# Performance work log

Hardware: AMD Instinct MI355X
Metric: run time of the kernel (lower is better)

Reference implementation:

```python
import jax, jax.numpy as jnp
import numpy as np

N = 100000          # num_nodes
E = 1250000         # num_edges
H = 64              # node_hidden_size
T = 2               # num_rounds


def setup_inputs() -> dict:
    key = jax.random.key(0)
    ks = jax.random.split(key, 10)
    s = 0.1  # init scale for weights
    return {
        "x": jax.random.normal(ks[0], (N, H), dtype=jnp.float32),
        "edge_index": jax.random.randint(ks[1], (2, E), 0, N, dtype=jnp.int64),
        "edge_attr": jax.random.normal(ks[2], (E, 1), dtype=jnp.float32),
        # message layers: Linear(2H+1 -> H), one per round
        "msg_W": jax.random.normal(ks[3], (T, H, 2 * H + 1), dtype=jnp.float32) * s,
        "msg_b": jax.random.normal(ks[4], (T, H), dtype=jnp.float32) * s,
        # GRUCell params, gate order (r, z, n) as in torch
        "gru_Wih": jax.random.normal(ks[5], (T, 3 * H, H), dtype=jnp.float32) * s,
        "gru_bih": jax.random.normal(ks[6], (T, 3 * H), dtype=jnp.float32) * s,
        "gru_Whh": jax.random.normal(ks[7], (T, 3 * H, H), dtype=jnp.float32) * s,
        "gru_bhh": jax.random.normal(ks[8], (T, 3 * H), dtype=jnp.float32) * s,
    }


def _gru_cell(inp, h, Wih, bih, Whh, bhh):
    # torch.nn.GRUCell math, gate order r, z, n
    gi = inp @ Wih.T + bih   # [N, 3H]
    gh = h @ Whh.T + bhh     # [N, 3H]
    i_r, i_z, i_n = jnp.split(gi, 3, axis=1)
    h_r, h_z, h_n = jnp.split(gh, 3, axis=1)
    r = jax.nn.sigmoid(i_r + h_r)
    z = jax.nn.sigmoid(i_z + h_z)
    n = jnp.tanh(i_n + r * h_n)
    return (1.0 - z) * n + z * h


def reference(x, edge_index, edge_attr, msg_W, msg_b, gru_Wih, gru_bih, gru_Whh, gru_bhh):
    row, col = edge_index[0], edge_index[1]
    num_rounds = msg_W.shape[0]
    for t in range(num_rounds):
        src = x[row]    # [E, H]
        dest = x[col]   # [E, H]
        m_input = jnp.concatenate([dest, src, edge_attr], axis=1)  # [E, 2H+1]
        messages = m_input @ msg_W[t].T + msg_b[t]                 # [E, H]
        agg = jax.ops.segment_sum(messages, row, num_segments=x.shape[0])  # [N, H]
        x = _gru_cell(agg, x, gru_Wih[t], gru_bih[t], gru_Whh[t], gru_bhh[t])
    return x
```

## Files before the change

### kernel.cpp

```cpp
#include <hip/hip_runtime.h>
#include <hip/hip_bf16.h>
#include <hip/hip_fp16.h>

#define H 64

typedef __attribute__((ext_vector_type(8))) short short8;
typedef __attribute__((ext_vector_type(4))) float float4v;

__device__ __forceinline__ float lane_bcast(float v, int k) {
    return __int_as_float(__builtin_amdgcn_readlane(__float_as_int(v), k));
}
__device__ __forceinline__ short f2bf_bits(float f) {
    union { __hip_bfloat16 b; short s; } u;
    u.b = __float2bfloat16(f);
    return u.s;
}
__device__ __forceinline__ float bf2f(unsigned short s) {
    union { unsigned int u; float f; } v;
    v.u = ((unsigned int)s) << 16;
    return v.f;
}
__device__ __forceinline__ void split8(const float* __restrict__ p,
                                       short8& hi, short8& lo) {
    float4v f0 = *(const float4v*)p;
    float4v f1 = *(const float4v*)(p + 4);
#pragma unroll
    for (int j = 0; j < 8; j++) {
        float f = (j < 4) ? f0[j] : f1[j - 4];
        short h = f2bf_bits(f);
        float fh = bf2f((unsigned short)h);
        hi[j] = h;
        lo[j] = f2bf_bits(f - fh);
    }
}
__device__ __forceinline__ void zero8(short8& hi, short8& lo) {
#pragma unroll
    for (int j = 0; j < 8; j++) { hi[j] = 0; lo[j] = 0; }
}

#define MFMA(a, b, c) __builtin_amdgcn_mfma_f32_16x16x32_bf16(a, b, c, 0, 0, 0)

__global__ __launch_bounds__(64) void prep_msg(
    const float* __restrict__ msg_W, short* __restrict__ frag)
{
    const int slot = blockIdx.x & 15, t = blockIdx.x >> 4, lane = threadIdx.x;
    const int tile = slot >> 1, ks = slot & 1;
    const float* W = msg_W + (size_t)t * H * 129;
    const int wrow = (tile & 3) * 16 + (lane & 15);
    const int coff = (tile < 4) ? 0 : 64;
    const int kq = (lane >> 4) * 8;
    short8 hi, lo;
    split8(W + (size_t)wrow * 129 + coff + ks * 32 + kq, hi, lo);
    short8* out = (short8*)(frag + (size_t)t * 16384);
    out[slot * 64 + lane] = hi;
    out[16 * 64 + slot * 64 + lane] = lo;
}

__global__ __launch_bounds__(64) void prep_gru(
    const float* __restrict__ Wih, const float* __restrict__ Whh,
    short* __restrict__ frag)
{
    const int slot = blockIdx.x % 48, t = blockIdx.x / 48, lane = threadIdx.x;
    const int tile = slot >> 1, ks = slot & 1;
    const int kq = (lane >> 4) * 8;
    const float* Wp = (tile < 12)
        ? (Wih + (size_t)t * 192 * H + ((size_t)(tile * 16 + (lane & 15))) * H)
        : (Whh + (size_t)t * 192 * H + ((size_t)((tile - 12) * 16 + (lane & 15))) * H);
    short8 hi, lo;
    split8(Wp + ks * 32 + kq, hi, lo);
    short8* out = (short8*)(frag + (size_t)t * 49152);
    out[slot * 64 + lane] = hi;
    out[48 * 64 + slot * 64 + lane] = lo;
}

__global__ __launch_bounds__(256) void count_kernel(
    const int* __restrict__ row, int* __restrict__ deg,
    int* __restrict__ lpos, int E)
{
    int e = blockIdx.x * 256 + threadIdx.x;
    if (e < E) lpos[e] = atomicAdd(&deg[row[e]], 1);
}

__global__ __launch_bounds__(256) void scan_block(
    const int* __restrict__ deg, int* __restrict__ offsets,
    int* __restrict__ block_sums, int N)
{
    __shared__ int s[256];
    int tid = threadIdx.x, gid = blockIdx.x * 256 + tid;
    int v = (gid < N) ? deg[gid] : 0;
    s[tid] = v; __syncthreads();
    for (int off = 1; off < 256; off <<= 1) {
        int t = (tid >= off) ? s[tid - off] : 0;
        __syncthreads();
        s[tid] += t;
        __syncthreads();
    }
    if (gid < N) offsets[gid] = s[tid] - v;
    if (tid == 255) block_sums[blockIdx.x] = s[255];
}

__global__ __launch_bounds__(512) void scan_sums(int* __restrict__ block_sums, int nb)
{
    __shared__ int s[512];
    int tid = threadIdx.x;
    int v = (tid < nb) ? block_sums[tid] : 0;
    s[tid] = v; __syncthreads();
    for (int off = 1; off < 512; off <<= 1) {
        int t = (tid >= off) ? s[tid - off] : 0;
        __syncthreads();
        s[tid] += t;
        __syncthreads();
    }
    if (tid < nb) block_sums[tid] = s[tid] - v;
}

__global__ __launch_bounds__(256) void scan_add(
    int* __restrict__ offsets, const int* __restrict__ block_sums, int N, int E)
{
    int gid = blockIdx.x * 256 + threadIdx.x;
    if (gid < N) offsets[gid] += block_sums[blockIdx.x];
    if (gid == 0) offsets[N] = E;
}

__global__ __launch_bounds__(256) void scatter_kernel(
    const int* __restrict__ row, const int* __restrict__ col,
    const float* __restrict__ attr, const int* __restrict__ offsets,
    const int* __restrict__ lpos, int2* __restrict__ edata, int E)
{
    int e = blockIdx.x * 256 + threadIdx.x;
    if (e < E) {
        int p = offsets[row[e]] + lpos[e];
        int2 v;
        v.x = col[e];
        v.y = __float_as_int(attr[e]);
        edata[p] = v;
    }
}

#define NSLOT(mt, ks, hl) ((((mt) * 2 + (ks)) * 2 + (hl)))
__global__ __launch_bounds__(256) void node_transform_mfma(
    const float* __restrict__ x, const short* __restrict__ frag,
    const float* __restrict__ b, const int* __restrict__ deg,
    __half* __restrict__ xd, float* __restrict__ agg, int N)
{
    __shared__ short8 afrag[16 * 64];
    const int tid = threadIdx.x, lane = tid & 63, q = tid >> 6;
    const int base = blockIdx.x * 64;
    const int arow = lane & 15;
    const int kq = (lane >> 4) * 8;
    const short8* fhi = (const short8*)frag;
    const short8* flo = fhi + 16 * 64;

    {
        const int m = base + q * 16 + arow;
#pragma unroll
        for (int ks = 0; ks < 2; ks++) {
            short8 hi, lo;
            if (m < N) split8(x + (size_t)m * H + ks * 32 + kq, hi, lo);
            else       zero8(hi, lo);
            afrag[NSLOT(q, ks, 0) * 64 + lane] = hi;
            afrag[NSLOT(q, ks, 1) * 64 + lane] = lo;
        }
    }
    __syncthreads();

    float4v accd[4], accs[4];
#pragma unroll
    for (int mt = 0; mt < 4; mt++) {
        accd[mt] = (float4v){0.f, 0.f, 0.f, 0.f};
        accs[mt] = (float4v){0.f, 0.f, 0.f, 0.f};
    }

#pragma unroll
    for (int ks = 0; ks < 2; ks++) {
        short8 ah[4], al[4];
#pragma unroll
        for (int mt = 0; mt < 4; mt++) {
            ah[mt] = afrag[NSLOT(mt, ks, 0) * 64 + lane];
            al[mt] = afrag[NSLOT(mt, ks, 1) * 64 + lane];
        }
        const int sd = q * 2 + ks;
        short8 bh = fhi[sd * 64 + lane];
        short8 bl = flo[sd * 64 + lane];
#pragma unroll
        for (int mt = 0; mt < 4; mt++) {
            accd[mt] = MFMA(ah[mt], bh, accd[mt]);
            accd[mt] = MFMA(al[mt], bh, accd[mt]);
            accd[mt] = MFMA(ah[mt], bl, accd[mt]);
        }
        const int ss = (4 + q) * 2 + ks;
        short8 ch = fhi[ss * 64 + lane];
        short8 cl = flo[ss * 64 + lane];
#pragma unroll
        for (int mt = 0; mt < 4; mt++) {
            accs[mt] = MFMA(ah[mt], ch, accs[mt]);
            accs[mt] = MFMA(al[mt], ch, accs[mt]);
            accs[mt] = MFMA(ah[mt], cl, accs[mt]);
        }
    }

    const int colb = lane & 15;
    const int rq4 = (lane >> 4) * 4;
    const int j = q * 16 + colb;
    const float bj = b[j];
#pragma unroll
    for (int mt = 0; mt < 4; mt++) {
#pragma unroll
        for (int r = 0; r < 4; r++) {
            const int m = base + mt * 16 + rq4 + r;
            if (m >= N) continue;
            xd[(size_t)m * H + j] = __float2half(accd[mt][r]);
            agg[(size_t)m * H + j] = (float)deg[m] * (accs[mt][r] + bj);
        }
    }
}

__global__ __launch_bounds__(256) void aggregate(
    const int* __restrict__ offsets, const int2* __restrict__ edata,
    const __half* __restrict__ xd,
    const float* __restrict__ W, float* __restrict__ agg, int N)
{
    const int tid = threadIdx.x, lane = tid & 63, wv = tid >> 6;
    const int n = blockIdx.x * 4 + wv;
    if (n >= N) return;
    const float wa = W[(size_t)lane * 129 + 128];
    const int beg = offsets[n], end = offsets[n + 1];
    float acc0 = agg[(size_t)n * H + lane];
    float acc1 = 0.f, acc2 = 0.f, acc3 = 0.f;
    for (int k = beg; k < end; k += 64) {
        int cnt = end - k; if (cnt > 64) cnt = 64;
        int2 ed = make_int2(0, 0);
        if (k + lane < end) ed = edata[k + lane];
        int j = 0;
        for (; j + 8 <= cnt; j += 8) {
            float v[8];
#pragma unroll
            for (int u = 0; u < 8; u++) {
                int c = __builtin_amdgcn_readlane(ed.x, j + u);
                v[u] = __half2float(xd[(size_t)c * H + lane]);
            }
#pragma unroll
            for (int u = 0; u < 8; u++) {
                float a = lane_bcast(__int_as_float(ed.y), j + u);
                float t = fmaf(wa, a, v[u]);
                if ((u & 3) == 0) acc0 += t;
                else if ((u & 3) == 1) acc1 += t;
                else if ((u & 3) == 2) acc2 += t;
                else acc3 += t;
            }
        }
        for (; j < cnt; j++) {
            int c = __builtin_amdgcn_readlane(ed.x, j);
            float a = lane_bcast(__int_as_float(ed.y), j);
            acc0 += fmaf(wa, a, __half2float(xd[(size_t)c * H + lane]));
        }
    }
    agg[(size_t)n * H + lane] = (acc0 + acc1) + (acc2 + acc3);
}

#define GSLOT(mt, ks, arr, hl) (((((mt) * 2 + (ks)) * 2 + (arr)) * 2 + (hl)))
__global__ __launch_bounds__(256) void gru_mfma(
    const float* __restrict__ agg, float* __restrict__ x,
    const short* __restrict__ frag,
    const float* __restrict__ bih, const float* __restrict__ bhh, int N)
{
    __shared__ short8 afrag[32 * 64];
    const int tid = threadIdx.x, lane = tid & 63, q = tid >> 6;
    const int base = blockIdx.x * 64;
    const int arow = lane & 15;
    const int kq = (lane >> 4) * 8;
    const short8* fhi = (const short8*)frag;
    const short8* flo = fhi + 48 * 64;

    {
        const int m = base + q * 16 + arow;
#pragma unroll
        for (int ks = 0; ks < 2; ks++) {
            short8 hi, lo;
            if (m < N) split8(agg + (size_t)m * H + ks * 32 + kq, hi, lo);
            else       zero8(hi, lo);
            afrag[GSLOT(q, ks, 0, 0) * 64 + lane] = hi;
            afrag[GSLOT(q, ks, 0, 1) * 64 + lane] = lo;
            if (m < N) split8(x + (size_t)m * H + ks * 32 + kq, hi, lo);
            else       zero8(hi, lo);
            afrag[GSLOT(q, ks, 1, 0) * 64 + lane] = hi;
            afrag[GSLOT(q, ks, 1, 1) * 64 + lane] = lo;
        }
    }
    __syncthreads();

    float4v acc[6][4];
#pragma unroll
    for (int g = 0; g < 6; g++)
#pragma unroll
        for (int mt = 0; mt < 4; mt++) acc[g][mt] = (float4v){0.f, 0.f, 0.f, 0.f};

#pragma unroll
    for (int ks = 0; ks < 2; ks++) {
        short8 ah[4], al[4];
#pragma unroll
        for (int mt = 0; mt < 4; mt++) {
            ah[mt] = afrag[GSLOT(mt, ks, 0, 0) * 64 + lane];
            al[mt] = afrag[GSLOT(mt, ks, 0, 1) * 64 + lane];
        }
#pragma unroll
        for (int g = 0; g < 3; g++) {
            const int si = (g * 4 + q) * 2 + ks;
            short8 bh = fhi[si * 64 + lane];
            short8 bl = flo[si * 64 + lane];
#pragma unroll
            for (int mt = 0; mt < 4; mt++) {
                acc[g][mt] = MFMA(ah[mt], bh, acc[g][mt]);
                acc[g][mt] = MFMA(al[mt], bh, acc[g][mt]);
                acc[g][mt] = MFMA(ah[mt], bl, acc[g][mt]);
            }
        }
#pragma unroll
        for (int mt = 0; mt < 4; mt++) {
            ah[mt] = afrag[GSLOT(mt, ks, 1, 0) * 64 + lane];
            al[mt] = afrag[GSLOT(mt, ks, 1, 1) * 64 + lane];
        }
#pragma unroll
        for (int g = 0; g < 3; g++) {
            const int sh = (12 + g * 4 + q) * 2 + ks;
            short8 bh = fhi[sh * 64 + lane];
            short8 bl = flo[sh * 64 + lane];
#pragma unroll
            for (int mt = 0; mt < 4; mt++) {
                acc[3 + g][mt] = MFMA(ah[mt], bh, acc[3 + g][mt]);
                acc[3 + g][mt] = MFMA(al[mt], bh, acc[3 + g][mt]);
                acc[3 + g][mt] = MFMA(ah[mt], bl, acc[3 + g][mt]);
            }
        }
    }

    const int colb = lane & 15;
    const int rq4 = (lane >> 4) * 4;
    const int j = q * 16 + colb;
    const float b_ir = bih[j], b_iz = bih[64 + j], b_in = bih[128 + j];
    const float b_hr = bhh[j], b_hz = bhh[64 + j], b_hn = bhh[128 + j];
#pragma unroll
    for (int mt = 0; mt < 4; mt++) {
#pragma unroll
        for (int r = 0; r < 4; r++) {
            const int m = base + mt * 16 + rq4 + r;
            if (m >= N) continue;
            float ir = acc[0][mt][r] + b_ir;
            float iz = acc[1][mt][r] + b_iz;
            float in_ = acc[2][mt][r] + b_in;
            float hr = acc[3][mt][r] + b_hr;
            float hz = acc[4][mt][r] + b_hz;
            float hn = acc[5][mt][r] + b_hn;
            float rr = 1.f / (1.f + __expf(-(ir + hr)));
            float zz = 1.f / (1.f + __expf(-(iz + hz)));
            float e2 = __expf(2.f * (in_ + rr * hn));
            float nn = 1.f - 2.f / (e2 + 1.f);
            float hold = x[(size_t)m * H + j];
            x[(size_t)m * H + j] = (1.f - zz) * nn + zz * hold;
        }
    }
}

extern "C" void kernel_launch(void* const* d_in, const int* in_sizes, int n_in,
                              void* d_out, int out_size, void* d_ws, size_t ws_size,
                              hipStream_t stream) {
    const float* x_in  = (const float*)d_in[0];
    const int*   ei    = (const int*)d_in[1];
    const float* attr  = (const float*)d_in[2];
    const float* msg_W = (const float*)d_in[3];
    const float* msg_b = (const float*)d_in[4];
    const float* Wih   = (const float*)d_in[5];
    const float* bih   = (const float*)d_in[6];
    const float* Whh   = (const float*)d_in[7];
    const float* bhh   = (const float*)d_in[8];

    const int N = in_sizes[0] / H;
    const int E = in_sizes[2];
    const int T = in_sizes[4] / H;
    const int* row = ei;
    const int* col = ei + E;

    float* x          = (float*)d_out;
    float* agg        = (float*)d_ws;
    __half* xd        = (__half*)(agg + (size_t)N * H);
    int*   deg        = (int*)(xd + (size_t)N * H);
    int*   offsets    = deg + N;
    int*   bsums      = offsets + (N + 1);
    int*   lpos       = bsums + 512;
    int2*  edata      = (int2*)(lpos + E);
    short* msgfrag    = (short*)(edata + E);
    short* grufrag    = msgfrag + (size_t)T * 16384;

    const int nb = (N + 255) / 256;
    const int eb = (E + 255) / 256;

    hipMemcpyAsync(x, x_in, (size_t)N * H * sizeof(float),
                   hipMemcpyDeviceToDevice, stream);
    hipMemsetAsync(deg, 0, (size_t)N * sizeof(int), stream);

    prep_msg<<<T * 16, 64, 0, stream>>>(msg_W, msgfrag);
    prep_gru<<<T * 48, 64, 0, stream>>>(Wih, Whh, grufrag);

    count_kernel<<<eb, 256, 0, stream>>>(row, deg, lpos, E);
    scan_block<<<nb, 256, 0, stream>>>(deg, offsets, bsums, N);
    scan_sums<<<1, 512, 0, stream>>>(bsums, nb);
    scan_add<<<nb, 256, 0, stream>>>(offsets, bsums, N, E);
    scatter_kernel<<<eb, 256, 0, stream>>>(row, col, attr, offsets, lpos,
                                           edata, E);

    const int nbq = (N + 63) / 64;
    const int agg_blocks = (N + 3) / 4;

    for (int t = 0; t < T; t++) {
        const float* Wt = msg_W + (size_t)t * H * (2 * H + 1);
        node_transform_mfma<<<nbq, 256, 0, stream>>>(
            x, msgfrag + (size_t)t * 16384, msg_b + (size_t)t * H, deg, xd, agg, N);
        aggregate<<<agg_blocks, 256, 0, stream>>>(
            offsets, edata, xd, Wt, agg, N);
        gru_mfma<<<nbq, 256, 0, stream>>>(
            agg, x, grufrag + (size_t)t * 49152,
            bih + (size_t)t * 3 * H, bhh + (size_t)t * 3 * H, N);
    }
}
```

Before: 385.2 us.

## Fuse setup kernels and chain GRU with next-round node transform

The edge-count kernel and the weight-fragment prep kernels are merged into one launch by partitioning blocks. The edge scatter, the x copy (replacing hipMemcpyAsync) and the first node transform are merged into a second launch. For all rounds but the last, the GRU update now also runs the next round's message node transform, reusing the freshly computed x held in LDS. This removes several launches and a global round-trip of x. In exchange the fused kernels use more registers and LDS and have branchy, heterogeneous blocks.

```diff
diff --git a/kernel.cpp b/kernel.cpp
--- a/kernel.cpp
+++ b/kernel.cpp
@@ -20,8 +20,7 @@
     v.u = ((unsigned int)s) << 16;
     return v.f;
 }
-__device__ __forceinline__ void split8(const float* __restrict__ p,
-                                       short8& hi, short8& lo) {
+__device__ __forceinline__ void split8(const float* p, short8& hi, short8& lo) {
     float4v f0 = *(const float4v*)p;
     float4v f1 = *(const float4v*)(p + 4);
 #pragma unroll
@@ -40,45 +39,47 @@
 
 #define MFMA(a, b, c) __builtin_amdgcn_mfma_f32_16x16x32_bf16(a, b, c, 0, 0, 0)
 
-__global__ __launch_bounds__(64) void prep_msg(
-    const float* __restrict__ msg_W, short* __restrict__ frag)
-{
-    const int slot = blockIdx.x & 15, t = blockIdx.x >> 4, lane = threadIdx.x;
-    const int tile = slot >> 1, ks = slot & 1;
-    const float* W = msg_W + (size_t)t * H * 129;
-    const int wrow = (tile & 3) * 16 + (lane & 15);
-    const int coff = (tile < 4) ? 0 : 64;
+__global__ __launch_bounds__(256) void count_prep(
+    const int* __restrict__ row, int* __restrict__ deg, int* __restrict__ lpos,
+    int E, int eb,
+    const float* __restrict__ msg_W, short* __restrict__ msgfrag,
+    const float* __restrict__ Wih, const float* __restrict__ Whh,
+    short* __restrict__ grufrag, int T)
+{
+    const int b = blockIdx.x;
+    if (b < eb) {
+        int e = b * 256 + threadIdx.x;
+        if (e < E) lpos[e] = atomicAdd(&deg[row[e]], 1);
+        return;
+    }
+    if (threadIdx.x >= 64) return;
+    int pb = b - eb;
+    const int lane = threadIdx.x;
     const int kq = (lane >> 4) * 8;
-    short8 hi, lo;
-    split8(W + (size_t)wrow * 129 + coff + ks * 32 + kq, hi, lo);
-    short8* out = (short8*)(frag + (size_t)t * 16384);
-    out[slot * 64 + lane] = hi;
-    out[16 * 64 + slot * 64 + lane] = lo;
-}
-
-__global__ __launch_bounds__(64) void prep_gru(
-    const float* __restrict__ Wih, const float* __restrict__ Whh,
-    short* __restrict__ frag)
-{
-    const int slot = blockIdx.x % 48, t = blockIdx.x / 48, lane = threadIdx.x;
-    const int tile = slot >> 1, ks = slot & 1;
-    const int kq = (lane >> 4) * 8;
-    const float* Wp = (tile < 12)
-        ? (Wih + (size_t)t * 192 * H + ((size_t)(tile * 16 + (lane & 15))) * H)
-        : (Whh + (size_t)t * 192 * H + ((size_t)((tile - 12) * 16 + (lane & 15))) * H);
-    short8 hi, lo;
-    split8(Wp + ks * 32 + kq, hi, lo);
-    short8* out = (short8*)(frag + (size_t)t * 49152);
-    out[slot * 64 + lane] = hi;
-    out[48 * 64 + slot * 64 + lane] = lo;
-}
-
-__global__ __launch_bounds__(256) void count_kernel(
-    const int* __restrict__ row, int* __restrict__ deg,
-    int* __restrict__ lpos, int E)
-{
-    int e = blockIdx.x * 256 + threadIdx.x;
-    if (e < E) lpos[e] = atomicAdd(&deg[row[e]], 1);
+    if (pb < T * 16) {
+        const int slot = pb & 15, t = pb >> 4;
+        const int tile = slot >> 1, ks = slot & 1;
+        const float* W = msg_W + (size_t)t * H * 129;
+        const int wrow = (tile & 3) * 16 + (lane & 15);
+        const int coff = (tile < 4) ? 0 : 64;
+        short8 hi, lo;
+        split8(W + (size_t)wrow * 129 + coff + ks * 32 + kq, hi, lo);
+        short8* out = (short8*)(msgfrag + (size_t)t * 16384);
+        out[slot * 64 + lane] = hi;
+        out[16 * 64 + slot * 64 + lane] = lo;
+    } else {
+        pb -= T * 16;
+        const int slot = pb % 48, t = pb / 48;
+        const int tile = slot >> 1, ks = slot & 1;
+        const float* Wp = (tile < 12)
+            ? (Wih + (size_t)t * 192 * H + ((size_t)(tile * 16 + (lane & 15))) * H)
+            : (Whh + (size_t)t * 192 * H + ((size_t)((tile - 12) * 16 + (lane & 15))) * H);
+        short8 hi, lo;
+        split8(Wp + ks * 32 + kq, hi, lo);
+        short8* out = (short8*)(grufrag + (size_t)t * 49152);
+        out[slot * 64 + lane] = hi;
+        out[48 * 64 + slot * 64 + lane] = lo;
+    }
 }
 
 __global__ __launch_bounds__(256) void scan_block(
@@ -122,41 +123,46 @@
     if (gid == 0) offsets[N] = E;
 }
 
-__global__ __launch_bounds__(256) void scatter_kernel(
+#define NSLOT(mt, ks, hl) ((((mt) * 2 + (ks)) * 2 + (hl)))
+__global__ __launch_bounds__(256) void scatter_nt0(
     const int* __restrict__ row, const int* __restrict__ col,
     const float* __restrict__ attr, const int* __restrict__ offsets,
-    const int* __restrict__ lpos, int2* __restrict__ edata, int E)
-{
-    int e = blockIdx.x * 256 + threadIdx.x;
-    if (e < E) {
-        int p = offsets[row[e]] + lpos[e];
-        int2 v;
-        v.x = col[e];
-        v.y = __float_as_int(attr[e]);
-        edata[p] = v;
-    }
-}
-
-#define NSLOT(mt, ks, hl) ((((mt) * 2 + (ks)) * 2 + (hl)))
-__global__ __launch_bounds__(256) void node_transform_mfma(
-    const float* __restrict__ x, const short* __restrict__ frag,
-    const float* __restrict__ b, const int* __restrict__ deg,
+    const int* __restrict__ lpos, int2* __restrict__ edata, int E, int eb,
+    const float* __restrict__ x_in, float* __restrict__ x,
+    const short* __restrict__ frag, const float* __restrict__ b,
+    const int* __restrict__ deg,
     __half* __restrict__ xd, float* __restrict__ agg, int N)
 {
     __shared__ short8 afrag[16 * 64];
+    if (blockIdx.x < eb) {
+        int e = blockIdx.x * 256 + threadIdx.x;
+        if (e < E) {
+            int p = offsets[row[e]] + lpos[e];
+            int2 v;
+            v.x = col[e];
+            v.y = __float_as_int(attr[e]);
+            edata[p] = v;
+        }
+        return;
+    }
     const int tid = threadIdx.x, lane = tid & 63, q = tid >> 6;
-    const int base = blockIdx.x * 64;
+    const int base = (blockIdx.x - eb) * 64;
     const int arow = lane & 15;
     const int kq = (lane >> 4) * 8;
     const short8* fhi = (const short8*)frag;
     const short8* flo = fhi + 16 * 64;
 
+    for (int i = tid; i < 64 * 64; i += 256) {
+        int m = base + (i >> 6);
+        if (m < N) x[(size_t)m * H + (i & 63)] = x_in[(size_t)m * H + (i & 63)];
+    }
+
     {
         const int m = base + q * 16 + arow;
 #pragma unroll
         for (int ks = 0; ks < 2; ks++) {
             short8 hi, lo;
-            if (m < N) split8(x + (size_t)m * H + ks * 32 + kq, hi, lo);
+            if (m < N) split8(x_in + (size_t)m * H + ks * 32 + kq, hi, lo);
             else       zero8(hi, lo);
             afrag[NSLOT(q, ks, 0) * 64 + lane] = hi;
             afrag[NSLOT(q, ks, 1) * 64 + lane] = lo;
@@ -170,7 +176,6 @@
         accd[mt] = (float4v){0.f, 0.f, 0.f, 0.f};
         accs[mt] = (float4v){0.f, 0.f, 0.f, 0.f};
     }
-
 #pragma unroll
     for (int ks = 0; ks < 2; ks++) {
         short8 ah[4], al[4];
@@ -259,6 +264,182 @@
 }
 
 #define GSLOT(mt, ks, arr, hl) (((((mt) * 2 + (ks)) * 2 + (arr)) * 2 + (hl)))
+__global__ __launch_bounds__(256) void gru_nt(
+    const float* __restrict__ agg_in, float* __restrict__ x,
+    const short* __restrict__ gfrag,
+    const float* __restrict__ bih, const float* __restrict__ bhh,
+    const short* __restrict__ mfrag, const float* __restrict__ mb,
+    const int* __restrict__ deg,
+    __half* __restrict__ xd, float* __restrict__ aggout, int N)
+{
+    __shared__ short8 lds[32 * 64];
+    const int tid = threadIdx.x, lane = tid & 63, q = tid >> 6;
+    const int base = blockIdx.x * 64;
+    const int arow = lane & 15;
+    const int kq = (lane >> 4) * 8;
+    const int colb = lane & 15;
+    const int rq4 = (lane >> 4) * 4;
+    const int j = q * 16 + colb;
+
+    {
+        const int m = base + q * 16 + arow;
+#pragma unroll
+        for (int ks = 0; ks < 2; ks++) {
+            short8 hi, lo;
+            if (m < N) split8(agg_in + (size_t)m * H + ks * 32 + kq, hi, lo);
+            else       zero8(hi, lo);
+            lds[GSLOT(q, ks, 0, 0) * 64 + lane] = hi;
+            lds[GSLOT(q, ks, 0, 1) * 64 + lane] = lo;
+            if (m < N) split8(x + (size_t)m * H + ks * 32 + kq, hi, lo);
+            else       zero8(hi, lo);
+            lds[GSLOT(q, ks, 1, 0) * 64 + lane] = hi;
+            lds[GSLOT(q, ks, 1, 1) * 64 + lane] = lo;
+        }
+    }
+    __syncthreads();
+
+    {
+        const short8* fhi = (const short8*)gfrag;
+        const short8* flo = fhi + 48 * 64;
+        float4v acc[6][4];
+#pragma unroll
+        for (int g = 0; g < 6; g++)
+#pragma unroll
+            for (int mt = 0; mt < 4; mt++) acc[g][mt] = (float4v){0.f, 0.f, 0.f, 0.f};
+
+#pragma unroll
+        for (int ks = 0; ks < 2; ks++) {
+            short8 ah[4], al[4];
+#pragma unroll
+            for (int mt = 0; mt < 4; mt++) {
+                ah[mt] = lds[GSLOT(mt, ks, 0, 0) * 64 + lane];
+                al[mt] = lds[GSLOT(mt, ks, 0, 1) * 64 + lane];
+            }
+#pragma unroll
+            for (int g = 0; g < 3; g++) {
+                const int si = (g * 4 + q) * 2 + ks;
+                short8 bh = fhi[si * 64 + lane];
+                short8 bl = flo[si * 64 + lane];
+#pragma unroll
+                for (int mt = 0; mt < 4; mt++) {
+                    acc[g][mt] = MFMA(ah[mt], bh, acc[g][mt]);
+                    acc[g][mt] = MFMA(al[mt], bh, acc[g][mt]);
+                    acc[g][mt] = MFMA(ah[mt], bl, acc[g][mt]);
+                }
+            }
+#pragma unroll
+            for (int mt = 0; mt < 4; mt++) {
+                ah[mt] = lds[GSLOT(mt, ks, 1, 0) * 64 + lane];
+                al[mt] = lds[GSLOT(mt, ks, 1, 1) * 64 + lane];
+            }
+#pragma unroll
+            for (int g = 0; g < 3; g++) {
+                const int sh = (12 + g * 4 + q) * 2 + ks;
+                short8 bh = fhi[sh * 64 + lane];
+                short8 bl = flo[sh * 64 + lane];
+#pragma unroll
+                for (int mt = 0; mt < 4; mt++) {
+                    acc[3 + g][mt] = MFMA(ah[mt], bh, acc[3 + g][mt]);
+                    acc[3 + g][mt] = MFMA(al[mt], bh, acc[3 + g][mt]);
+                    acc[3 + g][mt] = MFMA(ah[mt], bl, acc[3 + g][mt]);
+                }
+            }
+        }
+        __syncthreads();
+
+        float* xsh = (float*)lds;
+        const float b_ir = bih[j], b_iz = bih[64 + j], b_in = bih[128 + j];
+        const float b_hr = bhh[j], b_hz = bhh[64 + j], b_hn = bhh[128 + j];
+#pragma unroll
+        for (int mt = 0; mt < 4; mt++) {
+#pragma unroll
+            for (int r = 0; r < 4; r++) {
+                const int m = base + mt * 16 + rq4 + r;
+                if (m >= N) continue;
+                float ir = acc[0][mt][r] + b_ir;
+                float iz = acc[1][mt][r] + b_iz;
+                float in_ = acc[2][mt][r] + b_in;
+                float hr = acc[3][mt][r] + b_hr;
+                float hz = acc[4][mt][r] + b_hz;
+                float hn = acc[5][mt][r] + b_hn;
+                float rr = 1.f / (1.f + __expf(-(ir + hr)));
+                float zz = 1.f / (1.f + __expf(-(iz + hz)));
+                float e2 = __expf(2.f * (in_ + rr * hn));
+                float nn = 1.f - 2.f / (e2 + 1.f);
+                float hold = x[(size_t)m * H + j];
+                float xnew = (1.f - zz) * nn + zz * hold;
+                x[(size_t)m * H + j] = xnew;
+                xsh[(mt * 16 + rq4 + r) * 64 + j] = xnew;
+            }
+        }
+    }
+    __syncthreads();
+
+    {
+        float* xsh = (float*)lds;
+        short8* afragN = lds + 16 * 64;
+        {
+            const int m = base + q * 16 + arow;
+#pragma unroll
+            for (int ks = 0; ks < 2; ks++) {
+                short8 hi, lo;
+                if (m < N) split8(xsh + (q * 16 + arow) * 64 + ks * 32 + kq, hi, lo);
+                else       zero8(hi, lo);
+                afragN[NSLOT(q, ks, 0) * 64 + lane] = hi;
+                afragN[NSLOT(q, ks, 1) * 64 + lane] = lo;
+            }
+        }
+        __syncthreads();
+
+        const short8* fhi = (const short8*)mfrag;
+        const short8* flo = fhi + 16 * 64;
+        float4v accd[4], accs[4];
+#pragma unroll
+        for (int mt = 0; mt < 4; mt++) {
+            accd[mt] = (float4v){0.f, 0.f, 0.f, 0.f};
+            accs[mt] = (float4v){0.f, 0.f, 0.f, 0.f};
+        }
+#pragma unroll
+        for (int ks = 0; ks < 2; ks++) {
+            short8 ah[4], al[4];
+#pragma unroll
+            for (int mt = 0; mt < 4; mt++) {
+                ah[mt] = afragN[NSLOT(mt, ks, 0) * 64 + lane];
+                al[mt] = afragN[NSLOT(mt, ks, 1) * 64 + lane];
+            }
+            const int sd = q * 2 + ks;
+            short8 bh = fhi[sd * 64 + lane];
+            short8 bl = flo[sd * 64 + lane];
+#pragma unroll
+            for (int mt = 0; mt < 4; mt++) {
+                accd[mt] = MFMA(ah[mt], bh, accd[mt]);
+                accd[mt] = MFMA(al[mt], bh, accd[mt]);
+                accd[mt] = MFMA(ah[mt], bl, accd[mt]);
+            }
+            const int ss = (4 + q) * 2 + ks;
+            short8 ch = fhi[ss * 64 + lane];
+            short8 cl = flo[ss * 64 + lane];
+#pragma unroll
+            for (int mt = 0; mt < 4; mt++) {
+                accs[mt] = MFMA(ah[mt], ch, accs[mt]);
+                accs[mt] = MFMA(al[mt], ch, accs[mt]);
+                accs[mt] = MFMA(ah[mt], cl, accs[mt]);
+            }
+        }
+        const float bj = mb[j];
+#pragma unroll
+        for (int mt = 0; mt < 4; mt++) {
+#pragma unroll
+            for (int r = 0; r < 4; r++) {
+                const int m = base + mt * 16 + rq4 + r;
+                if (m >= N) continue;
+                xd[(size_t)m * H + j] = __float2half(accd[mt][r]);
+                aggout[(size_t)m * H + j] = (float)deg[m] * (accs[mt][r] + bj);
+            }
+        }
+    }
+}
+
 __global__ __launch_bounds__(256) void gru_mfma(
     const float* __restrict__ agg, float* __restrict__ x,
     const short* __restrict__ frag,
@@ -391,34 +572,35 @@
     short* msgfrag    = (short*)(edata + E);
     short* grufrag    = msgfrag + (size_t)T * 16384;
 
-    const int nb = (N + 255) / 256;
-    const int eb = (E + 255) / 256;
-
-    hipMemcpyAsync(x, x_in, (size_t)N * H * sizeof(float),
-                   hipMemcpyDeviceToDevice, stream);
+    const int nb  = (N + 255) / 256;
+    const int eb  = (E + 255) / 256;
+    const int nbq = (N + 63) / 64;
+    const int agg_blocks = (N + 3) / 4;
+
     hipMemsetAsync(deg, 0, (size_t)N * sizeof(int), stream);
 
-    prep_msg<<<T * 16, 64, 0, stream>>>(msg_W, msgfrag);
-    prep_gru<<<T * 48, 64, 0, stream>>>(Wih, Whh, grufrag);
-
-    count_kernel<<<eb, 256, 0, stream>>>(row, deg, lpos, E);
+    count_prep<<<eb + T * 16 + T * 48, 256, 0, stream>>>(
+        row, deg, lpos, E, eb, msg_W, msgfrag, Wih, Whh, grufrag, T);
     scan_block<<<nb, 256, 0, stream>>>(deg, offsets, bsums, N);
     scan_sums<<<1, 512, 0, stream>>>(bsums, nb);
     scan_add<<<nb, 256, 0, stream>>>(offsets, bsums, N, E);
-    scatter_kernel<<<eb, 256, 0, stream>>>(row, col, attr, offsets, lpos,
-                                           edata, E);
-
-    const int nbq = (N + 63) / 64;
-    const int agg_blocks = (N + 3) / 4;
+    scatter_nt0<<<eb + nbq, 256, 0, stream>>>(
+        row, col, attr, offsets, lpos, edata, E, eb,
+        x_in, x, msgfrag, msg_b, deg, xd, agg, N);
 
     for (int t = 0; t < T; t++) {
-        const float* Wt = msg_W + (size_t)t * H * (2 * H + 1);
-        node_transform_mfma<<<nbq, 256, 0, stream>>>(
-            x, msgfrag + (size_t)t * 16384, msg_b + (size_t)t * H, deg, xd, agg, N);
         aggregate<<<agg_blocks, 256, 0, stream>>>(
-            offsets, edata, xd, Wt, agg, N);
-        gru_mfma<<<nbq, 256, 0, stream>>>(
-            agg, x, grufrag + (size_t)t * 49152,
-            bih + (size_t)t * 3 * H, bhh + (size_t)t * 3 * H, N);
-    }
-}
+            offsets, edata, xd, msg_W + (size_t)t * H * 129, agg, N);
+        if (t + 1 < T) {
+            gru_nt<<<nbq, 256, 0, stream>>>(
+                agg, x, grufrag + (size_t)t * 49152,
+                bih + (size_t)t * 192, bhh + (size_t)t * 192,
+                msgfrag + (size_t)(t + 1) * 16384, msg_b + (size_t)(t + 1) * H,
+                deg, xd, agg, N);
+        } else {
+            gru_mfma<<<nbq, 256, 0, stream>>>(
+                agg, x, grufrag + (size_t)t * 49152,
+                bih + (size_t)t * 192, bhh + (size_t)t * 192, N);
+        }
+    }
+}
```

Result: no change. 391.1 us (+1.5%).
